# Performance work log

Hardware: AMD Instinct MI355X
Metric: run time of the kernel (lower is better)

## Reference

```python
import jax, jax.numpy as jnp
import numpy as np


def _fake_quant(x, num_bits):
    # Per-tensor uniform min/max fake quantization with STE (straight-through).
    qmax = float(2 ** num_bits - 1)
    mn = jnp.min(x)
    mx = jnp.max(x)
    scale = (mx - mn) / qmax
    q = jnp.round((x - mn) / scale) * scale + mn
    return x + jax.lax.stop_gradient(q - x)


def _qlinear(x, W, b, num_bits):
    xq = _fake_quant(x, num_bits)
    Wq = _fake_quant(W, num_bits)
    return xq @ Wq.T + b


def setup_inputs() -> dict:
    key = jax.random.key(0)
    ks = jax.random.split(key, 7)
    B, D, H = 8192, 1024, 1024
    s = 1.0 / np.sqrt(H)
    return {
        "input": jax.random.normal(ks[0], (B, D), jnp.float32),
        "h": jax.random.normal(ks[1], (B, H), jnp.float32),
        "c": jax.random.normal(ks[2], (B, H), jnp.float32),
        "W_in": jax.random.normal(ks[3], (4 * H, D), jnp.float32) * s,
        "b_in": jax.random.normal(ks[4], (4 * H,), jnp.float32) * s,
        "W_h": jax.random.normal(ks[5], (4 * H, H), jnp.float32) * s,
        "b_h": jax.random.normal(ks[6], (4 * H,), jnp.float32) * s,
        "num_bits": 8,
        "num_bits_grad": 8,
    }


def reference(input, h, c, W_in, b_in, W_h, b_h, num_bits, num_bits_grad):
    B = input.shape[0]
    Hd = h.shape[1]
    mixed_input = _qlinear(input, W_in, b_in, num_bits).reshape(B, 4, Hd)
    mixed_hidden = _qlinear(h, W_h, b_h, num_bits).reshape(B, 4, Hd)
    gates = mixed_input + mixed_hidden  # [B, 4, H]
    i = jax.nn.sigmoid(gates[:, 0, :])
    f = jax.nn.sigmoid(gates[:, 1, :])
    g = jnp.tanh(gates[:, 2, :])
    o = jax.nn.sigmoid(gates[:, 3, :])
    c_ = f * c + i * g
    h_ = o * jnp.tanh(c_)
    return (h_, c_)
```

## Files before the change

### kernel.cpp

```cpp
#include <hip/hip_runtime.h>
#include <hip/hip_bf16.h>

typedef unsigned short u16;
typedef int i32x4 __attribute__((ext_vector_type(4)));
typedef signed char s8;

#define NB_RED 256

__global__ void k_minmax_partial(const float* __restrict__ x, const float* __restrict__ h,
                                 const float* __restrict__ wi, const float* __restrict__ wh,
                                 float* __restrict__ partials) {
    int t = blockIdx.y;
    const float* p = (t == 0) ? x : (t == 1) ? h : (t == 2) ? wi : wh;
    int n4 = ((t < 2) ? (8192 * 1024) : (4096 * 1024)) >> 2;
    float mn = 3.4e38f, mx = -3.4e38f;
    const float4* p4 = (const float4*)p;
    for (int i = blockIdx.x * blockDim.x + threadIdx.x; i < n4; i += gridDim.x * blockDim.x) {
        float4 v = p4[i];
        mn = fminf(mn, fminf(fminf(v.x, v.y), fminf(v.z, v.w)));
        mx = fmaxf(mx, fmaxf(fmaxf(v.x, v.y), fmaxf(v.z, v.w)));
    }
    for (int d = 1; d < 64; d <<= 1) {
        mn = fminf(mn, __shfl_xor(mn, d));
        mx = fmaxf(mx, __shfl_xor(mx, d));
    }
    __shared__ float smn[4], smx[4];
    int wv = threadIdx.x >> 6;
    if ((threadIdx.x & 63) == 0) { smn[wv] = mn; smx[wv] = mx; }
    __syncthreads();
    if (threadIdx.x == 0) {
        mn = fminf(fminf(smn[0], smn[1]), fminf(smn[2], smn[3]));
        mx = fmaxf(fmaxf(smx[0], smx[1]), fmaxf(smx[2], smx[3]));
        partials[(t * NB_RED + blockIdx.x) * 2 + 0] = mn;
        partials[(t * NB_RED + blockIdx.x) * 2 + 1] = mx;
    }
}

__global__ void k_minmax_final(const float* __restrict__ partials, const int* __restrict__ nbits,
                               float* __restrict__ params) {
    int t = blockIdx.x;
    int tid = threadIdx.x;
    float mn = partials[(t * NB_RED + tid) * 2 + 0];
    float mx = partials[(t * NB_RED + tid) * 2 + 1];
    for (int d = 1; d < 64; d <<= 1) {
        mn = fminf(mn, __shfl_xor(mn, d));
        mx = fmaxf(mx, __shfl_xor(mx, d));
    }
    __shared__ float smn[4], smx[4];
    int wv = tid >> 6;
    if ((tid & 63) == 0) { smn[wv] = mn; smx[wv] = mx; }
    __syncthreads();
    if (tid == 0) {
        mn = fminf(fminf(smn[0], smn[1]), fminf(smn[2], smn[3]));
        mx = fmaxf(fmaxf(smx[0], smx[1]), fmaxf(smx[2], smx[3]));
        float qmax = (float)((1u << (*nbits)) - 1u);
        params[t * 2 + 0] = mn;
        params[t * 2 + 1] = (mx - mn) / qmax;
    }
}

static __device__ __forceinline__ int block_reduce_i(int v, int tid) {
    for (int d = 1; d < 64; d <<= 1) v += __shfl_xor(v, d);
    __shared__ int sred[4];
    if ((tid & 63) == 0) sred[tid >> 6] = v;
    __syncthreads();
    return sred[0] + sred[1] + sred[2] + sred[3];
}

__global__ void k_quant(const float* __restrict__ x, const float* __restrict__ h,
                        const float* __restrict__ wi, const float* __restrict__ wh,
                        const float* __restrict__ params,
                        const float* __restrict__ b_in, const float* __restrict__ b_h,
                        s8* __restrict__ A8, s8* __restrict__ W8,
                        float* __restrict__ Rax, float* __restrict__ Rah,
                        float* __restrict__ Rbi, float* __restrict__ Rbh,
                        float* __restrict__ bc) {
    int b = blockIdx.x;
    int t = threadIdx.x;
    if (b < 16384) {
        int tsel = b >> 13;
        int row = b & 8191;
        const float* src = tsel ? h : x;
        float mn = params[tsel * 2 + 0], s = params[tsel * 2 + 1];
        float4 v = ((const float4*)(src + (size_t)row * 1024))[t];
        int k0 = (int)fminf(255.f, fmaxf(0.f, rintf((v.x - mn) / s)));
        int k1 = (int)fminf(255.f, fmaxf(0.f, rintf((v.y - mn) / s)));
        int k2 = (int)fminf(255.f, fmaxf(0.f, rintf((v.z - mn) / s)));
        int k3 = (int)fminf(255.f, fmaxf(0.f, rintf((v.w - mn) / s)));
        unsigned p = ((unsigned)((k0 - 128) & 0xff)) | ((unsigned)((k1 - 128) & 0xff) << 8) |
                     ((unsigned)((k2 - 128) & 0xff) << 16) | ((unsigned)((k3 - 128) & 0xff) << 24);
        *(unsigned*)(A8 + (size_t)row * 2048 + tsel * 1024 + t * 4) = p;
        int sum = block_reduce_i(k0 + k1 + k2 + k3 - 512, t);
        if (t == 0) (tsel ? Rah : Rax)[row] = (float)sum;
    } else if (b < 24576) {
        int bb = b - 16384;
        int tsel = bb >> 12;
        int row = bb & 4095;
        const float* src = tsel ? wh : wi;
        float mn = params[(2 + tsel) * 2 + 0], s = params[(2 + tsel) * 2 + 1];
        int g = row >> 10, j = row & 1023;
        int prow = (j >> 4) * 64 + g * 16 + (j & 15);
        float4 v = ((const float4*)(src + (size_t)row * 1024))[t];
        int k0 = (int)fminf(255.f, fmaxf(0.f, rintf((v.x - mn) / s)));
        int k1 = (int)fminf(255.f, fmaxf(0.f, rintf((v.y - mn) / s)));
        int k2 = (int)fminf(255.f, fmaxf(0.f, rintf((v.z - mn) / s)));
        int k3 = (int)fminf(255.f, fmaxf(0.f, rintf((v.w - mn) / s)));
        unsigned p = ((unsigned)((k0 - 128) & 0xff)) | ((unsigned)((k1 - 128) & 0xff) << 8) |
                     ((unsigned)((k2 - 128) & 0xff) << 16) | ((unsigned)((k3 - 128) & 0xff) << 24);
        *(unsigned*)(W8 + (size_t)prow * 2048 + tsel * 1024 + t * 4) = p;
        int sum = block_reduce_i(k0 + k1 + k2 + k3 - 512, t);
        if (t == 0) (tsel ? Rbh : Rbi)[prow] = (float)sum;
    } else {
        int n = (b - 24576) * 256 + t;
        int j = (n >> 6) * 16 + (n & 15);
        int g = (n >> 4) & 3;
        bc[n] = b_in[g * 1024 + j] + b_h[g * 1024 + j];
    }
}

__global__ __launch_bounds__(512, 4) void k_gemm_lstm(
    const s8* __restrict__ A8, const s8* __restrict__ W8,
    const float* __restrict__ params, const float* __restrict__ bc,
    const float* __restrict__ Rax, const float* __restrict__ Rah,
    const float* __restrict__ Rbi, const float* __restrict__ Rbh,
    const float* __restrict__ c_in, float* __restrict__ out) {
    __shared__ __align__(16) s8 As[3][8192];
    __shared__ __align__(16) s8 Bs[3][16384];

    const int tid = threadIdx.x;
    const int wave = tid >> 6, lane = tid & 63;
    const int wr = wave >> 2, wc = wave & 3;
    const int la = lane & 15, hi = lane >> 4;

    const int bid = blockIdx.x;
    const int l = bid >> 3;
    const int bx = l >> 3;
    const int by = (bid & 7) * 8 + (l & 7);
    const int bm = by * 128, bn = bx * 256;

    const int skb = (((tid & 3) ^ ((tid >> 3) & 3)) * 16);
    const int rx = ((hi ^ ((la >> 1) & 3)) * 16);

    const float sa = params[1], sh = params[3], si = params[5], sw = params[7];
    const float csx = sa * si, csh = sh * sw;
    const float r = csx / csh;

    const s8* pA0 = A8 + (size_t)(bm + (tid >> 2)) * 2048 + skb;
    const s8* pB0 = W8 + (size_t)(bn + (tid >> 2)) * 2048 + skb;
    const s8* pB1 = pB0 + (size_t)128 * 2048;

    i32x4 acc[4][4];
#pragma unroll
    for (int m = 0; m < 4; m++)
#pragma unroll
        for (int n = 0; n < 4; n++) acc[m][n] = (i32x4)0;

#define STAGE(B, T)                                                                               \
    do {                                                                                          \
        __builtin_amdgcn_global_load_lds(                                                         \
            (const __attribute__((address_space(1))) void*)(pA0 + (T) * 64),                      \
            (__attribute__((address_space(3))) void*)&As[(B)][tid * 16], 16, 0, 0);               \
        __builtin_amdgcn_global_load_lds(                                                         \
            (const __attribute__((address_space(1))) void*)(pB0 + (T) * 64),                      \
            (__attribute__((address_space(3))) void*)&Bs[(B)][tid * 16], 16, 0, 0);               \
        __builtin_amdgcn_global_load_lds(                                                         \
            (const __attribute__((address_space(1))) void*)(pB1 + (T) * 64),                      \
            (__attribute__((address_space(3))) void*)&Bs[(B)][8192 + tid * 16], 16, 0, 0);        \
    } while (0)

#define COMPUTE(B)                                                                                \
    do {                                                                                          \
        i32x4 af[4], bf[4];                                                                       \
        _Pragma("unroll") for (int m = 0; m < 4; m++)                                             \
            af[m] = *(const i32x4*)&As[(B)][(wr * 64 + m * 16 + la) * 64 + rx];                   \
        _Pragma("unroll") for (int n = 0; n < 4; n++)                                             \
            bf[n] = *(const i32x4*)&Bs[(B)][(wc * 64 + n * 16 + la) * 64 + rx];                   \
        _Pragma("unroll") for (int m = 0; m < 4; m++)                                             \
            _Pragma("unroll") for (int n = 0; n < 4; n++)                                         \
                acc[m][n] = __builtin_amdgcn_mfma_i32_16x16x64_i8(af[m], bf[n], acc[m][n], 0, 0, 0); \
    } while (0)

    STAGE(0, 0);
    STAGE(1, 1);
    asm volatile("s_waitcnt vmcnt(3)" ::: "memory");
    __builtin_amdgcn_s_barrier();

#pragma unroll
    for (int t = 0; t < 32; ++t) {
        if (t < 30) STAGE((t + 2) % 3, t + 2);
        if (t == 16) {
#pragma unroll
            for (int m = 0; m < 4; m++)
#pragma unroll
                for (int n = 0; n < 4; n++)
#pragma unroll
                    for (int q = 0; q < 4; q++)
                        acc[m][n][q] = (int)rintf((float)acc[m][n][q] * r);
        }
        COMPUTE(t % 3);
        if (t < 30) { asm volatile("s_waitcnt vmcnt(3)" ::: "memory"); }
        else if (t == 30) { asm volatile("s_waitcnt vmcnt(0)" ::: "memory"); }
        if (t < 31) __builtin_amdgcn_s_barrier();
    }

#undef STAGE
#undef COMPUTE

    float mna = params[0], mnh = params[2], mni = params[4], mnw = params[6];
    float za = mna + 128.0f * sa, zi = mni + 128.0f * si;
    float zh = mnh + 128.0f * sh, zw = mnw + 128.0f * sw;
    float C0 = 1024.0f * (za * zi + zh * zw);
    float cax = sa * zi, cah = sh * zw;
    float cbx = si * za, cbh = sw * zh;

    const int nb = bn + wc * 64;
    float colt[4];
#pragma unroll
    for (int g = 0; g < 4; ++g) {
        int np = nb + g * 16 + la;
        colt[g] = bc[np] + cbx * Rbi[np] + cbh * Rbh[np] + C0;
    }
    const int ub = (nb >> 6) * 16 + la;

#pragma unroll
    for (int m = 0; m < 4; m++) {
#pragma unroll
        for (int q = 0; q < 4; q++) {
            int row = bm + wr * 64 + m * 16 + 4 * hi + q;
            float rterm = cax * Rax[row] + cah * Rah[row];
            float g0 = colt[0] + rterm + csh * (float)acc[m][0][q];
            float g1 = colt[1] + rterm + csh * (float)acc[m][1][q];
            float g2 = colt[2] + rterm + csh * (float)acc[m][2][q];
            float g3 = colt[3] + rterm + csh * (float)acc[m][3][q];
            float iv = 1.0f / (1.0f + __expf(-g0));
            float fv = 1.0f / (1.0f + __expf(-g1));
            float gv = tanhf(g2);
            float ov = 1.0f / (1.0f + __expf(-g3));
            size_t off = (size_t)row * 1024 + ub;
            float cv = c_in[off];
            float cn = fv * cv + iv * gv;
            float hn = ov * tanhf(cn);
            out[off] = hn;
            out[(size_t)8192 * 1024 + off] = cn;
        }
    }
}

extern "C" void kernel_launch(void* const* d_in, const int* in_sizes, int n_in,
                              void* d_out, int out_size, void* d_ws, size_t ws_size,
                              hipStream_t stream) {
    const float* x = (const float*)d_in[0];
    const float* h = (const float*)d_in[1];
    const float* c = (const float*)d_in[2];
    const float* wi = (const float*)d_in[3];
    const float* bi = (const float*)d_in[4];
    const float* wh = (const float*)d_in[5];
    const float* bh = (const float*)d_in[6];
    const int* nbits = (const int*)d_in[7];
    float* out = (float*)d_out;

    char* ws = (char*)d_ws;
    float* params   = (float*)ws;
    float* partials = (float*)(ws + 64);
    float* bc  = (float*)(ws + 16384);
    float* Rax = (float*)(ws + 32768);
    float* Rah = (float*)(ws + 65536);
    float* Rbi = (float*)(ws + 98304);
    float* Rbh = (float*)(ws + 114688);
    s8* A8 = (s8*)(ws + 131072);
    s8* W8 = (s8*)(ws + 131072 + (size_t)16 * 1024 * 1024);

    k_minmax_partial<<<dim3(NB_RED, 4), 256, 0, stream>>>(x, h, wi, wh, partials);
    k_minmax_final<<<4, 256, 0, stream>>>(partials, nbits, params);
    k_quant<<<24592, 256, 0, stream>>>(x, h, wi, wh, params, bi, bh,
                                       A8, W8, Rax, Rah, Rbi, Rbh, bc);
    k_gemm_lstm<<<1024, 512, 0, stream>>>(A8, W8, params, bc, Rax, Rah, Rbi, Rbh, c, out);
}
```

Before: 133.1 us.

## Switch int8 GEMM to 32x32x32 MFMA tiles with matching weight permutation

Replaces the 16x16x64 int8 MFMA tiling with 32x32x32 MFMA. Each wave now covers a 32-row by 128-column slab and keeps four 16-element accumulators, so the weight/bias row permutation moves to 32-wide gate groups and the LDS read swizzle and epilogue index mapping are rewritten to match. The larger instruction is meant to raise the number of accumulate operations per LDS operand read. It also replaces tanhf with an exp-based fast tanh, which saves transcendental cost but may lose accuracy or overflow for large inputs.

After: 136.8 us. 2.8% more time.

```diff
diff --git a/kernel.cpp b/kernel.cpp
--- a/kernel.cpp
+++ b/kernel.cpp
@@ -3,9 +3,15 @@
 
 typedef unsigned short u16;
 typedef int i32x4 __attribute__((ext_vector_type(4)));
+typedef int i32x16 __attribute__((ext_vector_type(16)));
 typedef signed char s8;
 
 #define NB_RED 256
+
+static __device__ __forceinline__ float tanh_fast(float x) {
+    float t = __expf(2.0f * x);
+    return 1.0f - 2.0f / (t + 1.0f);
+}
 
 __global__ void k_minmax_partial(const float* __restrict__ x, const float* __restrict__ h,
                                  const float* __restrict__ wi, const float* __restrict__ wh,
@@ -99,7 +105,7 @@
         const float* src = tsel ? wh : wi;
         float mn = params[(2 + tsel) * 2 + 0], s = params[(2 + tsel) * 2 + 1];
         int g = row >> 10, j = row & 1023;
-        int prow = (j >> 4) * 64 + g * 16 + (j & 15);
+        int prow = (j >> 5) * 128 + g * 32 + (j & 31);
         float4 v = ((const float4*)(src + (size_t)row * 1024))[t];
         int k0 = (int)fminf(255.f, fmaxf(0.f, rintf((v.x - mn) / s)));
         int k1 = (int)fminf(255.f, fmaxf(0.f, rintf((v.y - mn) / s)));
@@ -112,8 +118,8 @@
         if (t == 0) (tsel ? Rbh : Rbi)[prow] = (float)sum;
     } else {
         int n = (b - 24576) * 256 + t;
-        int j = (n >> 6) * 16 + (n & 15);
-        int g = (n >> 4) & 3;
+        int j = (n >> 7) * 32 + (n & 31);
+        int g = (n >> 5) & 3;
         bc[n] = b_in[g * 1024 + j] + b_h[g * 1024 + j];
     }
 }
@@ -129,8 +135,8 @@
 
     const int tid = threadIdx.x;
     const int wave = tid >> 6, lane = tid & 63;
-    const int wr = wave >> 2, wc = wave & 3;
-    const int la = lane & 15, hi = lane >> 4;
+    const int wr = wave >> 1, wc = wave & 1;
+    const int l31 = lane & 31, lh = lane >> 5;
 
     const int bid = blockIdx.x;
     const int l = bid >> 3;
@@ -139,7 +145,7 @@
     const int bm = by * 128, bn = bx * 256;
 
     const int skb = (((tid & 3) ^ ((tid >> 3) & 3)) * 16);
-    const int rx = ((hi ^ ((la >> 1) & 3)) * 16);
+    const int q = (l31 >> 1) & 3;
 
     const float sa = params[1], sh = params[3], si = params[5], sw = params[7];
     const float csx = sa * si, csh = sh * sw;
@@ -149,11 +155,9 @@
     const s8* pB0 = W8 + (size_t)(bn + (tid >> 2)) * 2048 + skb;
     const s8* pB1 = pB0 + (size_t)128 * 2048;
 
-    i32x4 acc[4][4];
-#pragma unroll
-    for (int m = 0; m < 4; m++)
-#pragma unroll
-        for (int n = 0; n < 4; n++) acc[m][n] = (i32x4)0;
+    i32x16 acc[4];
+#pragma unroll
+    for (int f = 0; f < 4; f++) acc[f] = (i32x16)0;
 
 #define STAGE(B, T)                                                                               \
     do {                                                                                          \
@@ -170,14 +174,15 @@
 
 #define COMPUTE(B)                                                                                \
     do {                                                                                          \
-        i32x4 af[4], bf[4];                                                                       \
-        _Pragma("unroll") for (int m = 0; m < 4; m++)                                             \
-            af[m] = *(const i32x4*)&As[(B)][(wr * 64 + m * 16 + la) * 64 + rx];                   \
-        _Pragma("unroll") for (int n = 0; n < 4; n++)                                             \
-            bf[n] = *(const i32x4*)&Bs[(B)][(wc * 64 + n * 16 + la) * 64 + rx];                   \
-        _Pragma("unroll") for (int m = 0; m < 4; m++)                                             \
-            _Pragma("unroll") for (int n = 0; n < 4; n++)                                         \
-                acc[m][n] = __builtin_amdgcn_mfma_i32_16x16x64_i8(af[m], bf[n], acc[m][n], 0, 0, 0); \
+        _Pragma("unroll") for (int ks = 0; ks < 2; ++ks) {                                        \
+            const int ro = ((ks * 2 + lh) ^ q) * 16;                                              \
+            i32x4 a = *(const i32x4*)&As[(B)][(wr * 32 + l31) * 64 + ro];                         \
+            i32x4 bf;                                                                             \
+            _Pragma("unroll") for (int f = 0; f < 4; ++f) {                                       \
+                bf = *(const i32x4*)&Bs[(B)][(wc * 128 + f * 32 + l31) * 64 + ro];                \
+                acc[f] = __builtin_amdgcn_mfma_i32_32x32x32_i8(a, bf, acc[f], 0, 0, 0);           \
+            }                                                                                     \
+        }                                                                                         \
     } while (0)
 
     STAGE(0, 0);
@@ -190,12 +195,10 @@
         if (t < 30) STAGE((t + 2) % 3, t + 2);
         if (t == 16) {
 #pragma unroll
-            for (int m = 0; m < 4; m++)
-#pragma unroll
-                for (int n = 0; n < 4; n++)
-#pragma unroll
-                    for (int q = 0; q < 4; q++)
-                        acc[m][n][q] = (int)rintf((float)acc[m][n][q] * r);
+            for (int f = 0; f < 4; f++)
+#pragma unroll
+                for (int e = 0; e < 16; e++)
+                    acc[f][e] = (int)rintf((float)acc[f][e] * r);
         }
         COMPUTE(t % 3);
         if (t < 30) { asm volatile("s_waitcnt vmcnt(3)" ::: "memory"); }
@@ -213,36 +216,33 @@
     float cax = sa * zi, cah = sh * zw;
     float cbx = si * za, cbh = sw * zh;
 
-    const int nb = bn + wc * 64;
+    const int nb = bn + wc * 128;
     float colt[4];
 #pragma unroll
-    for (int g = 0; g < 4; ++g) {
-        int np = nb + g * 16 + la;
-        colt[g] = bc[np] + cbx * Rbi[np] + cbh * Rbh[np] + C0;
-    }
-    const int ub = (nb >> 6) * 16 + la;
-
-#pragma unroll
-    for (int m = 0; m < 4; m++) {
-#pragma unroll
-        for (int q = 0; q < 4; q++) {
-            int row = bm + wr * 64 + m * 16 + 4 * hi + q;
-            float rterm = cax * Rax[row] + cah * Rah[row];
-            float g0 = colt[0] + rterm + csh * (float)acc[m][0][q];
-            float g1 = colt[1] + rterm + csh * (float)acc[m][1][q];
-            float g2 = colt[2] + rterm + csh * (float)acc[m][2][q];
-            float g3 = colt[3] + rterm + csh * (float)acc[m][3][q];
-            float iv = 1.0f / (1.0f + __expf(-g0));
-            float fv = 1.0f / (1.0f + __expf(-g1));
-            float gv = tanhf(g2);
-            float ov = 1.0f / (1.0f + __expf(-g3));
-            size_t off = (size_t)row * 1024 + ub;
-            float cv = c_in[off];
-            float cn = fv * cv + iv * gv;
-            float hn = ov * tanhf(cn);
-            out[off] = hn;
-            out[(size_t)8192 * 1024 + off] = cn;
-        }
+    for (int f = 0; f < 4; ++f) {
+        int np = nb + f * 32 + l31;
+        colt[f] = bc[np] + cbx * Rbi[np] + cbh * Rbh[np] + C0;
+    }
+    const int ub = (nb >> 7) * 32 + l31;
+
+#pragma unroll
+    for (int reg = 0; reg < 16; reg++) {
+        int row = bm + wr * 32 + (reg & 3) + 8 * (reg >> 2) + 4 * lh;
+        float rterm = cax * Rax[row] + cah * Rah[row];
+        float g0 = colt[0] + rterm + csh * (float)acc[0][reg];
+        float g1 = colt[1] + rterm + csh * (float)acc[1][reg];
+        float g2 = colt[2] + rterm + csh * (float)acc[2][reg];
+        float g3 = colt[3] + rterm + csh * (float)acc[3][reg];
+        float iv = 1.0f / (1.0f + __expf(-g0));
+        float fv = 1.0f / (1.0f + __expf(-g1));
+        float gv = tanh_fast(g2);
+        float ov = 1.0f / (1.0f + __expf(-g3));
+        size_t off = (size_t)row * 1024 + ub;
+        float cv = c_in[off];
+        float cn = fv * cv + iv * gv;
+        float hn = ov * tanh_fast(cn);
+        out[off] = hn;
+        out[(size_t)8192 * 1024 + off] = cn;
     }
 }
 
```
